# Optimization experiments

Measured on AMD Instinct MI355X. Metric: run time of the kernel, lower is better.

Reference implementation:

```python
import jax, jax.numpy as jnp
import numpy as np

B, S, D_IN, HID, H, OUT = 4, 2048, 1024, 1024, 16, 128
DH = HID // H
SCALE = float(np.sqrt(DH))
ELEV, FLOOR2 = 4, 32


def setup_inputs() -> dict:
    key = jax.random.key(0)
    ks = jax.random.split(key, 12)
    w = lambda k, o, i: jax.random.normal(k, (o, i), dtype=jnp.float32) * 0.02
    b = lambda k, o: jax.random.normal(k, (o,), dtype=jnp.float32) * 0.02
    return {
        "query": jax.random.normal(ks[0], (B, S, D_IN), dtype=jnp.float32),
        "key": jax.random.normal(ks[1], (B, S, D_IN), dtype=jnp.float32),
        "value": jax.random.normal(ks[2], (B, S, D_IN), dtype=jnp.float32),
        "mask": jax.random.randint(ks[3], (B, 1, 1, S), 0, 2, dtype=jnp.int32),
        "wq_w": w(ks[4], HID, D_IN), "wq_b": b(ks[5], HID),
        "wk_w": w(ks[6], HID, D_IN), "wk_b": b(ks[7], HID),
        "wv_w": w(ks[8], HID, D_IN), "wv_b": b(ks[9], HID),
        "fc_w": w(ks[10], OUT, HID), "fc_b": b(ks[11], OUT),
    }


def reference(query, key, value, mask, wq_w, wq_b, wk_w, wk_b, wv_w, wv_b, fc_w, fc_b):
    bsz, seq = query.shape[0], query.shape[1]
    # torch Linear: x @ W.T + b
    split = lambda x: x.reshape(bsz, seq, H, DH).transpose(0, 2, 1, 3)  # (b,h,s,dh)
    Q = split(query @ wq_w.T + wq_b)
    K = split(key @ wk_w.T + wk_b)
    V = split(value @ wv_w.T + wv_b)
    energy = jnp.einsum('bhqd,bhkd->bhqk', Q, K) / SCALE
    energy = jnp.where(mask == 0, jnp.float32(-1e10), energy)
    attn = jax.nn.softmax(energy, axis=-1)  # dropout is identity in eval mode
    x = jnp.einsum('bhqk,bhkd->bhqd', attn, V)
    x = x.transpose(0, 2, 1, 3).reshape(bsz, seq, HID)
    x = x @ fc_w.T + fc_b
    x = x.reshape(-1, ELEV, FLOOR2)  # (b*s, elevator_num, floor_num*2)
    return jax.nn.softmax(x, axis=1)  # nn.Softmax(dim=1)
```

## Files before the change

### kernel.cpp

```cpp
#include <hip/hip_runtime.h>
#include <stdint.h>

#define S_LEN 2048
#define DK 1024
#define NH 16
#define DH 64
#define LOG2E 1.4426950408889634f
#define M_FIX 10.0f

typedef __attribute__((ext_vector_type(8))) short bf16x8;
typedef __attribute__((ext_vector_type(4))) float f32x4;

__device__ __forceinline__ unsigned short f2bf(float f) {
    union { float f; uint32_t u; } v; v.f = f;
    return (unsigned short)((v.u + 0x7fffu + ((v.u >> 16) & 1u)) >> 16);
}

__device__ __forceinline__ float fast_exp2(float x) {
#if __has_builtin(__builtin_amdgcn_exp2f)
    return __builtin_amdgcn_exp2f(x);
#else
    return exp2f(x);
#endif
}

__device__ __forceinline__ uint32_t cvt_pk_bf16(float a, float b) {
    uint32_t r;
    asm("v_cvt_pk_bf16_f32 %0, %1, %2" : "=v"(r) : "v"(a), "v"(b));
    return r;
}

__device__ __forceinline__ void gload_lds16(const void* g, void* l) {
    __builtin_amdgcn_global_load_lds((const __attribute__((address_space(1))) void*)g,
                                     (__attribute__((address_space(3))) void*)l, 16, 0, 0);
}

__global__ __launch_bounds__(256) void cvt3_kernel(
    const float* __restrict__ a0, const float* __restrict__ a1, const float* __restrict__ a2,
    unsigned short* __restrict__ o0, unsigned short* __restrict__ o1, unsigned short* __restrict__ o2,
    int n4)
{
    const float* in = (blockIdx.y == 0) ? a0 : ((blockIdx.y == 1) ? a1 : a2);
    unsigned short* out = (blockIdx.y == 0) ? o0 : ((blockIdx.y == 1) ? o1 : o2);
    const float4* pin = (const float4*)in;
    ushort4* pout = (ushort4*)out;
    int i = blockIdx.x * blockDim.x + threadIdx.x;
    int stride = gridDim.x * blockDim.x;
    for (; i < n4; i += stride) {
        float4 v = pin[i];
        ushort4 o;
        o.x = f2bf(v.x); o.y = f2bf(v.y); o.z = f2bf(v.z); o.w = f2bf(v.w);
        pout[i] = o;
    }
}

__global__ __launch_bounds__(256) void cvt4_kernel(
    const float* __restrict__ a0, const float* __restrict__ a1,
    const float* __restrict__ a2, const float* __restrict__ a3,
    unsigned short* __restrict__ o0, unsigned short* __restrict__ o1,
    unsigned short* __restrict__ o2, unsigned short* __restrict__ o3,
    int n4_012, int n4_3)
{
    const int y = blockIdx.y;
    const float* in = (y == 0) ? a0 : ((y == 1) ? a1 : ((y == 2) ? a2 : a3));
    unsigned short* out = (y == 0) ? o0 : ((y == 1) ? o1 : ((y == 2) ? o2 : o3));
    const int n4 = (y == 3) ? n4_3 : n4_012;
    const float4* pin = (const float4*)in;
    ushort4* pout = (ushort4*)out;
    int i = blockIdx.x * blockDim.x + threadIdx.x;
    int stride = gridDim.x * blockDim.x;
    for (; i < n4; i += stride) {
        float4 v = pin[i];
        ushort4 o;
        o.x = f2bf(v.x); o.y = f2bf(v.y); o.z = f2bf(v.z); o.w = f2bf(v.w);
        pout[i] = o;
    }
}

__global__ __launch_bounds__(256) void proj_gemm(
    const unsigned short* __restrict__ Xq, const unsigned short* __restrict__ Xk, const unsigned short* __restrict__ Xv,
    const unsigned short* __restrict__ Wq, const unsigned short* __restrict__ Wk, const unsigned short* __restrict__ Wv,
    const float* __restrict__ bq, const float* __restrict__ bk, const float* __restrict__ bv,
    unsigned short* __restrict__ Qh, unsigned short* __restrict__ Kh, unsigned short* __restrict__ Vt)
{
    const int d = blockIdx.x + (blockIdx.y << 3) + (blockIdx.z << 9);
    const int k = d & 7, s = d >> 3;
    const int nn = s & 7;
    const int mz = ((s >> 3) << 3) + k;
    const int m0 = (mz & 63) * 128;
    const int z = mz >> 6;

    const unsigned short* X = (z == 0) ? Xq : ((z == 1) ? Xk : Xv);
    const unsigned short* W = (z == 0) ? Wq : ((z == 1) ? Wk : Wv);
    const float* bias = (z == 0) ? bq : ((z == 1) ? bk : bv);

    const int n0 = nn * 128;
    const int tid = threadIdx.x;
    const int w = tid >> 6;
    const int l = tid & 63;
    const int wm = w >> 1, wn = w & 1;
    const int g = l >> 4, c = l & 15;

    __shared__ __align__(16) unsigned short As[3][128 * 32];
    __shared__ __align__(16) unsigned short Bs[3][128 * 32];

    f32x4 acc[4][4] = {};

    const int srow = l >> 2;
    const int schunk = (((l & 3) - (l >> 3)) & 3) * 8;

    auto stage = [&](int kk, int buf) {
#pragma unroll
        for (int j = 0; j < 2; ++j) {
            int r0 = 32 * w + 16 * j;
            gload_lds16(X + (size_t)(m0 + r0 + srow) * DK + kk + schunk, &As[buf][r0 * 32]);
            gload_lds16(W + (size_t)(n0 + r0 + srow) * DK + kk + schunk, &Bs[buf][r0 * 32]);
        }
    };

    stage(0, 0);
    stage(32, 1);

    int cur = 0;
    for (int step = 0; step < 32; ++step) {
        if (step < 31) asm volatile("s_waitcnt vmcnt(4)" ::: "memory");
        else           asm volatile("s_waitcnt vmcnt(0)" ::: "memory");
        __builtin_amdgcn_s_barrier();
        __builtin_amdgcn_sched_barrier(0);

        if (step < 30) {
            int nb = cur + 2; if (nb >= 3) nb -= 3;
            stage((step + 2) << 5, nb);
        }

        bf16x8 a[4], bb[4];
        const int rchunk = 8 * ((g + (c >> 1)) & 3);
#pragma unroll
        for (int mi = 0; mi < 4; ++mi)
            a[mi] = *(const bf16x8*)&As[cur][(64 * wm + 16 * mi + c) * 32 + rchunk];
#pragma unroll
        for (int nj = 0; nj < 4; ++nj)
            bb[nj] = *(const bf16x8*)&Bs[cur][(64 * wn + 16 * nj + c) * 32 + rchunk];
        __builtin_amdgcn_s_setprio(1);
#pragma unroll
        for (int mi = 0; mi < 4; ++mi)
#pragma unroll
            for (int nj = 0; nj < 4; ++nj)
                acc[mi][nj] = __builtin_amdgcn_mfma_f32_16x16x32_bf16(a[mi], bb[nj], acc[mi][nj], 0, 0, 0);
        __builtin_amdgcn_s_setprio(0);

        ++cur; if (cur == 3) cur = 0;
    }

    const float scale = (z == 0) ? 0.125f : 1.0f;
#pragma unroll
    for (int mi = 0; mi < 4; ++mi) {
#pragma unroll
        for (int nj = 0; nj < 4; ++nj) {
            int col = n0 + 64 * wn + 16 * nj + c;
            float bval = bias[col];
            int h = col >> 6, dh = col & 63;
            int row0 = m0 + 64 * wm + 16 * mi + 4 * g;
            int b = row0 >> 11, ss = row0 & 2047;
            if (z != 2) {
                unsigned short* Out = (z == 0) ? Qh : Kh;
#pragma unroll
                for (int r = 0; r < 4; ++r) {
                    float v = (acc[mi][nj][r] + bval) * scale;
                    Out[((size_t)(b * NH + h) * S_LEN + (ss + r)) * DH + dh] = f2bf(v);
                }
            } else {
                ushort4 o;
                o.x = f2bf(acc[mi][nj][0] + bval);
                o.y = f2bf(acc[mi][nj][1] + bval);
                o.z = f2bf(acc[mi][nj][2] + bval);
                o.w = f2bf(acc[mi][nj][3] + bval);
                int q = (ss >> 2) & 7;
                int newpos = (ss & ~31) + 8 * (q & 3) + 4 * (q >> 2);
                *(ushort4*)&Vt[((size_t)(b * NH + h) * DH + dh) * S_LEN + newpos] = o;
            }
        }
    }
}

__global__ __launch_bounds__(256, 5) void attn_kernel(
    const unsigned short* __restrict__ Qh, const unsigned short* __restrict__ Kh,
    const unsigned short* __restrict__ Vt, const int* __restrict__ maskI,
    unsigned short* __restrict__ O)
{
    const int id = blockIdx.x + (blockIdx.y << 4);
    const int swzid = (id & 7) * 128 + (id >> 3);
    const int q0 = (swzid & 15) * 128;
    const int bh = swzid >> 4;
    const int b = bh >> 4, h = bh & 15;
    const int tid = threadIdx.x, w = tid >> 6, l = tid & 63;
    const int g = l >> 4, c = l & 15;

    __shared__ __align__(16) unsigned short Ks[2][32 * 64];
    __shared__ __align__(16) unsigned short Vs[2][64 * 32];
    __shared__ __align__(16) float mskA[S_LEN];

    bf16x8 qf[2][2];
    const size_t qbase = (size_t)bh * S_LEN + q0 + 32 * w;
#pragma unroll
    for (int mi = 0; mi < 2; ++mi)
#pragma unroll
        for (int k32 = 0; k32 < 2; ++k32)
            qf[mi][k32] = *(const bf16x8*)&Qh[(qbase + 16 * mi + c) * DH + k32 * 32 + 8 * g];

    f32x4 ao[2][4] = {};
    f32x4 ls[2] = {};
    bf16x8 ones;
#pragma unroll
    for (int j = 0; j < 8; ++j) ones[j] = (short)0x3F80;

    const int kswz = ((l & 7) ^ (l >> 3)) * 8;
    const int vrow = l >> 2;
    const int vsrc = (((l & 3) - (l >> 3)) & 3) * 8;

    gload_lds16(Kh + ((size_t)bh * S_LEN + 8 * w + (l >> 3)) * DH + kswz, &Ks[0][w * 512]);
    gload_lds16(Vt + ((size_t)bh * DH + 16 * w + vrow) * S_LEN + vsrc, &Vs[0][w * 512]);
    {
        const int4* mp = (const int4*)(maskI + b * S_LEN);
#pragma unroll
        for (int i = 0; i < 2; ++i) {
            int idx = tid + 256 * i;
            int4 m = mp[idx];
            float4 f;
            f.x = m.x ? (-M_FIX * LOG2E) : -3e38f;
            f.y = m.y ? (-M_FIX * LOG2E) : -3e38f;
            f.z = m.z ? (-M_FIX * LOG2E) : -3e38f;
            f.w = m.w ? (-M_FIX * LOG2E) : -3e38f;
            *(float4*)&mskA[idx * 4] = f;
        }
    }

    for (int t = 0; t < 64; ++t) {
        const int cur = t & 1;
        const int kv0 = t << 5;
        __syncthreads();

        if (t < 63) {
            int kvn = kv0 + 32;
            gload_lds16(Kh + ((size_t)bh * S_LEN + kvn + 8 * w + (l >> 3)) * DH + kswz, &Ks[cur ^ 1][w * 512]);
            gload_lds16(Vt + ((size_t)bh * DH + 16 * w + vrow) * S_LEN + kvn + vsrc, &Vs[cur ^ 1][w * 512]);
        }

        f32x4 sf[2][2] = {};
        __builtin_amdgcn_s_setprio(1);
#pragma unroll
        for (int nj = 0; nj < 2; ++nj) {
            int krow = 16 * nj + c;
#pragma unroll
            for (int k32 = 0; k32 < 2; ++k32) {
                int chunk = (k32 * 4 + g) ^ (krow & 7);
                bf16x8 kf = *(const bf16x8*)&Ks[cur][krow * 64 + chunk * 8];
#pragma unroll
                for (int mi = 0; mi < 2; ++mi)
                    sf[mi][nj] = __builtin_amdgcn_mfma_f32_16x16x32_bf16(kf, qf[mi][k32], sf[mi][nj], 0, 0, 0);
            }
        }
        __builtin_amdgcn_s_setprio(0);

        float4 mk0 = *(const float4*)&mskA[kv0 + 4 * g];
        float4 mk1 = *(const float4*)&mskA[kv0 + 16 + 4 * g];
        bf16x8 pf[2];
#pragma unroll
        for (int mi = 0; mi < 2; ++mi) {
            float e00 = fast_exp2(fmaf(sf[mi][0][0], LOG2E, mk0.x));
            float e01 = fast_exp2(fmaf(sf[mi][0][1], LOG2E, mk0.y));
            float e02 = fast_exp2(fmaf(sf[mi][0][2], LOG2E, mk0.z));
            float e03 = fast_exp2(fmaf(sf[mi][0][3], LOG2E, mk0.w));
            float e10 = fast_exp2(fmaf(sf[mi][1][0], LOG2E, mk1.x));
            float e11 = fast_exp2(fmaf(sf[mi][1][1], LOG2E, mk1.y));
            float e12 = fast_exp2(fmaf(sf[mi][1][2], LOG2E, mk1.z));
            float e13 = fast_exp2(fmaf(sf[mi][1][3], LOG2E, mk1.w));
            union { uint32_t u[4]; bf16x8 v; } pu;
            pu.u[0] = cvt_pk_bf16(e00, e01);
            pu.u[1] = cvt_pk_bf16(e02, e03);
            pu.u[2] = cvt_pk_bf16(e10, e11);
            pu.u[3] = cvt_pk_bf16(e12, e13);
            pf[mi] = pu.v;
        }

        __builtin_amdgcn_s_setprio(1);
#pragma unroll
        for (int nc = 0; nc < 4; ++nc) {
            int row = 16 * nc + c;
            int s16 = (g + (c >> 1)) & 3;
            bf16x8 vf = *(const bf16x8*)&Vs[cur][row * 32 + 8 * s16];
#pragma unroll
            for (int mi = 0; mi < 2; ++mi)
                ao[mi][nc] = __builtin_amdgcn_mfma_f32_16x16x32_bf16(pf[mi], vf, ao[mi][nc], 0, 0, 0);
        }
#pragma unroll
        for (int mi = 0; mi < 2; ++mi)
            ls[mi] = __builtin_amdgcn_mfma_f32_16x16x32_bf16(pf[mi], ones, ls[mi], 0, 0, 0);
        __builtin_amdgcn_s_setprio(0);
    }

#pragma unroll
    for (int mi = 0; mi < 2; ++mi)
#pragma unroll
        for (int r = 0; r < 4; ++r) {
            int s = q0 + 32 * w + 16 * mi + 4 * g + r;
            float inv = 1.0f / ls[mi][r];
#pragma unroll
            for (int nc = 0; nc < 4; ++nc) {
                int dh = 16 * nc + c;
                O[(size_t)(b * S_LEN + s) * 1024 + h * DH + dh] = f2bf(ao[mi][nc][r] * inv);
            }
        }
}

__global__ __launch_bounds__(256) void fc_kernel(
    const unsigned short* __restrict__ O, const unsigned short* __restrict__ Wf,
    const float* __restrict__ bfc, float* __restrict__ out)
{
    const int m0 = blockIdx.x * 64;
    const int tid = threadIdx.x, w = tid >> 6, l = tid & 63;
    const int g = l >> 4, c = l & 15;

    __shared__ __align__(16) unsigned short As[3][64 * 32];
    __shared__ __align__(16) unsigned short Bs[3][128 * 32];

    f32x4 acc[8] = {};

    const int srow = l >> 2;
    const int schunk = (((l & 3) - (l >> 3)) & 3) * 8;

    auto stage = [&](int kk, int buf) {
        gload_lds16(O + (size_t)(m0 + 16 * w + srow) * DK + kk + schunk, &As[buf][16 * w * 32]);
#pragma unroll
        for (int j = 0; j < 2; ++j) {
            int r0 = 32 * w + 16 * j;
            gload_lds16(Wf + (size_t)(r0 + srow) * DK + kk + schunk, &Bs[buf][r0 * 32]);
        }
    };

    stage(0, 0);
    stage(32, 1);

    int cur = 0;
    for (int step = 0; step < 32; ++step) {
        if (step < 31) asm volatile("s_waitcnt vmcnt(3)" ::: "memory");
        else           asm volatile("s_waitcnt vmcnt(0)" ::: "memory");
        __builtin_amdgcn_s_barrier();
        __builtin_amdgcn_sched_barrier(0);

        if (step < 30) {
            int nb = cur + 2; if (nb >= 3) nb -= 3;
            stage((step + 2) << 5, nb);
        }

        const int rchunk = 8 * ((g + (c >> 1)) & 3);
        bf16x8 a = *(const bf16x8*)&As[cur][(16 * w + c) * 32 + rchunk];
        bf16x8 bb[8];
#pragma unroll
        for (int nj = 0; nj < 8; ++nj)
            bb[nj] = *(const bf16x8*)&Bs[cur][(16 * nj + c) * 32 + rchunk];
        __builtin_amdgcn_s_setprio(1);
#pragma unroll
        for (int nj = 0; nj < 8; ++nj)
            acc[nj] = __builtin_amdgcn_mfma_f32_16x16x32_bf16(a, bb[nj], acc[nj], 0, 0, 0);
        __builtin_amdgcn_s_setprio(0);

        ++cur; if (cur == 3) cur = 0;
    }

#pragma unroll
    for (int r = 0; r < 4; ++r) {
        int row = m0 + 16 * w + (l >> 4) * 4 + r;
#pragma unroll
        for (int par = 0; par < 2; ++par) {
            float v[4];
#pragma unroll
            for (int e = 0; e < 4; ++e) {
                int col = 16 * (2 * e + par) + (l & 15);
                v[e] = acc[2 * e + par][r] + bfc[col];
            }
            float mx = fmaxf(fmaxf(v[0], v[1]), fmaxf(v[2], v[3]));
            float ex[4], ssum = 0.f;
#pragma unroll
            for (int e = 0; e < 4; ++e) { ex[e] = fast_exp2((v[e] - mx) * LOG2E); ssum += ex[e]; }
            float inv = 1.0f / ssum;
#pragma unroll
            for (int e = 0; e < 4; ++e) {
                int col = 16 * (2 * e + par) + (l & 15);
                out[(size_t)row * 128 + col] = ex[e] * inv;
            }
        }
    }
}

extern "C" void kernel_launch(void* const* d_in, const int* in_sizes, int n_in,
                              void* d_out, int out_size, void* d_ws, size_t ws_size,
                              hipStream_t stream) {
    (void)in_sizes; (void)n_in; (void)out_size; (void)ws_size;
    const float* q    = (const float*)d_in[0];
    const float* k    = (const float*)d_in[1];
    const float* v    = (const float*)d_in[2];
    const int*   mask = (const int*)d_in[3];
    const float* wq_w = (const float*)d_in[4];
    const float* wq_b = (const float*)d_in[5];
    const float* wk_w = (const float*)d_in[6];
    const float* wk_b = (const float*)d_in[7];
    const float* wv_w = (const float*)d_in[8];
    const float* wv_b = (const float*)d_in[9];
    const float* fc_w = (const float*)d_in[10];
    const float* fc_b = (const float*)d_in[11];

    const size_t NX = (size_t)8192 * 1024;
    const size_t NW = (size_t)1024 * 1024;
    const size_t NF = (size_t)128 * 1024;

    unsigned short* Xq = (unsigned short*)d_ws;
    unsigned short* Xk = Xq + NX;
    unsigned short* Xv = Xk + NX;
    unsigned short* Wq = Xv + NX;
    unsigned short* Wk = Wq + NW;
    unsigned short* Wv = Wk + NW;
    unsigned short* Wf = Wv + NW;
    unsigned short* Qh = Wf + NF;
    unsigned short* Kh = Qh + NX;
    unsigned short* Vt = Kh + NX;
    unsigned short* O  = Xq;

    cvt3_kernel<<<dim3(2048, 3), 256, 0, stream>>>(q, k, v, Xq, Xk, Xv, (int)(NX / 4));
    cvt4_kernel<<<dim3(512, 4), 256, 0, stream>>>(wq_w, wk_w, wv_w, fc_w,
                                                  Wq, Wk, Wv, Wf,
                                                  (int)(NW / 4), (int)(NF / 4));

    proj_gemm<<<dim3(8, 64, 3), 256, 0, stream>>>(Xq, Xk, Xv, Wq, Wk, Wv,
                                                  wq_b, wk_b, wv_b, Qh, Kh, Vt);
    attn_kernel<<<dim3(16, 64), 256, 0, stream>>>(Qh, Kh, Vt, mask, O);
    fc_kernel<<<128, 256, 0, stream>>>(O, Wf, fc_b, (float*)d_out);
}
```

Before: 195.2 us.

## Merge conversion kernels, shrink B staging, and fold log2e and mask into MFMA

Three independent changes. The two fp32-to-bf16 conversion launches become one 7-slice launch, removing a kernel launch and its tail. In the projection GEMM the weight tile is double-buffered instead of triple-buffered and prefetched one step ahead, which cuts LDS use at the cost of a shallower prefetch for B. The Q projection now folds log2(e) into its scale and the attention kernel seeds the MFMA accumulator with the mask bias, so the per-element fma before exp2 goes away; slightly different rounding of Q in bf16 is the tradeoff.

```diff
diff --git a/kernel.cpp b/kernel.cpp
--- a/kernel.cpp
+++ b/kernel.cpp
@@ -35,36 +35,21 @@
                                      (__attribute__((address_space(3))) void*)l, 16, 0, 0);
 }
 
-__global__ __launch_bounds__(256) void cvt3_kernel(
+__global__ __launch_bounds__(256) void cvt7_kernel(
     const float* __restrict__ a0, const float* __restrict__ a1, const float* __restrict__ a2,
+    const float* __restrict__ a3, const float* __restrict__ a4, const float* __restrict__ a5,
+    const float* __restrict__ a6,
     unsigned short* __restrict__ o0, unsigned short* __restrict__ o1, unsigned short* __restrict__ o2,
-    int n4)
-{
-    const float* in = (blockIdx.y == 0) ? a0 : ((blockIdx.y == 1) ? a1 : a2);
-    unsigned short* out = (blockIdx.y == 0) ? o0 : ((blockIdx.y == 1) ? o1 : o2);
-    const float4* pin = (const float4*)in;
-    ushort4* pout = (ushort4*)out;
-    int i = blockIdx.x * blockDim.x + threadIdx.x;
-    int stride = gridDim.x * blockDim.x;
-    for (; i < n4; i += stride) {
-        float4 v = pin[i];
-        ushort4 o;
-        o.x = f2bf(v.x); o.y = f2bf(v.y); o.z = f2bf(v.z); o.w = f2bf(v.w);
-        pout[i] = o;
-    }
-}
-
-__global__ __launch_bounds__(256) void cvt4_kernel(
-    const float* __restrict__ a0, const float* __restrict__ a1,
-    const float* __restrict__ a2, const float* __restrict__ a3,
-    unsigned short* __restrict__ o0, unsigned short* __restrict__ o1,
-    unsigned short* __restrict__ o2, unsigned short* __restrict__ o3,
-    int n4_012, int n4_3)
+    unsigned short* __restrict__ o3, unsigned short* __restrict__ o4, unsigned short* __restrict__ o5,
+    unsigned short* __restrict__ o6,
+    int n4_big, int n4_w, int n4_f)
 {
     const int y = blockIdx.y;
-    const float* in = (y == 0) ? a0 : ((y == 1) ? a1 : ((y == 2) ? a2 : a3));
-    unsigned short* out = (y == 0) ? o0 : ((y == 1) ? o1 : ((y == 2) ? o2 : o3));
-    const int n4 = (y == 3) ? n4_3 : n4_012;
+    const float* in = (y == 0) ? a0 : (y == 1) ? a1 : (y == 2) ? a2 :
+                      (y == 3) ? a3 : (y == 4) ? a4 : (y == 5) ? a5 : a6;
+    unsigned short* out = (y == 0) ? o0 : (y == 1) ? o1 : (y == 2) ? o2 :
+                          (y == 3) ? o3 : (y == 4) ? o4 : (y == 5) ? o5 : o6;
+    const int n4 = (y < 3) ? n4_big : ((y < 6) ? n4_w : n4_f);
     const float4* pin = (const float4*)in;
     ushort4* pout = (ushort4*)out;
     int i = blockIdx.x * blockDim.x + threadIdx.x;
@@ -102,45 +87,53 @@
     const int g = l >> 4, c = l & 15;
 
     __shared__ __align__(16) unsigned short As[3][128 * 32];
-    __shared__ __align__(16) unsigned short Bs[3][128 * 32];
+    __shared__ __align__(16) unsigned short Bs[2][128 * 32];
 
     f32x4 acc[4][4] = {};
 
     const int srow = l >> 2;
     const int schunk = (((l & 3) - (l >> 3)) & 3) * 8;
 
-    auto stage = [&](int kk, int buf) {
+    auto stageA = [&](int kk, int buf) {
 #pragma unroll
         for (int j = 0; j < 2; ++j) {
             int r0 = 32 * w + 16 * j;
             gload_lds16(X + (size_t)(m0 + r0 + srow) * DK + kk + schunk, &As[buf][r0 * 32]);
+        }
+    };
+    auto stageB = [&](int kk, int buf) {
+#pragma unroll
+        for (int j = 0; j < 2; ++j) {
+            int r0 = 32 * w + 16 * j;
             gload_lds16(W + (size_t)(n0 + r0 + srow) * DK + kk + schunk, &Bs[buf][r0 * 32]);
         }
     };
 
-    stage(0, 0);
-    stage(32, 1);
-
-    int cur = 0;
+    stageA(0, 0);
+    stageB(0, 0);
+    stageA(32, 1);
+
+    int curA = 0;
     for (int step = 0; step < 32; ++step) {
-        if (step < 31) asm volatile("s_waitcnt vmcnt(4)" ::: "memory");
+        if (step < 31) asm volatile("s_waitcnt vmcnt(2)" ::: "memory");
         else           asm volatile("s_waitcnt vmcnt(0)" ::: "memory");
         __builtin_amdgcn_s_barrier();
         __builtin_amdgcn_sched_barrier(0);
 
+        if (step < 31) stageB((step + 1) << 5, (step + 1) & 1);
         if (step < 30) {
-            int nb = cur + 2; if (nb >= 3) nb -= 3;
-            stage((step + 2) << 5, nb);
+            int nb = curA + 2; if (nb >= 3) nb -= 3;
+            stageA((step + 2) << 5, nb);
         }
 
         bf16x8 a[4], bb[4];
         const int rchunk = 8 * ((g + (c >> 1)) & 3);
 #pragma unroll
         for (int mi = 0; mi < 4; ++mi)
-            a[mi] = *(const bf16x8*)&As[cur][(64 * wm + 16 * mi + c) * 32 + rchunk];
+            a[mi] = *(const bf16x8*)&As[curA][(64 * wm + 16 * mi + c) * 32 + rchunk];
 #pragma unroll
         for (int nj = 0; nj < 4; ++nj)
-            bb[nj] = *(const bf16x8*)&Bs[cur][(64 * wn + 16 * nj + c) * 32 + rchunk];
+            bb[nj] = *(const bf16x8*)&Bs[step & 1][(64 * wn + 16 * nj + c) * 32 + rchunk];
         __builtin_amdgcn_s_setprio(1);
 #pragma unroll
         for (int mi = 0; mi < 4; ++mi)
@@ -149,10 +142,10 @@
                 acc[mi][nj] = __builtin_amdgcn_mfma_f32_16x16x32_bf16(a[mi], bb[nj], acc[mi][nj], 0, 0, 0);
         __builtin_amdgcn_s_setprio(0);
 
-        ++cur; if (cur == 3) cur = 0;
-    }
-
-    const float scale = (z == 0) ? 0.125f : 1.0f;
+        ++curA; if (curA == 3) curA = 0;
+    }
+
+    const float scale = (z == 0) ? (0.125f * LOG2E) : 1.0f;
 #pragma unroll
     for (int mi = 0; mi < 4; ++mi) {
 #pragma unroll
@@ -246,7 +239,14 @@
             gload_lds16(Vt + ((size_t)bh * DH + 16 * w + vrow) * S_LEN + kvn + vsrc, &Vs[cur ^ 1][w * 512]);
         }
 
-        f32x4 sf[2][2] = {};
+        float4 mk0 = *(const float4*)&mskA[kv0 + 4 * g];
+        float4 mk1 = *(const float4*)&mskA[kv0 + 16 + 4 * g];
+        f32x4 sf[2][2];
+        sf[0][0] = f32x4{mk0.x, mk0.y, mk0.z, mk0.w};
+        sf[1][0] = sf[0][0];
+        sf[0][1] = f32x4{mk1.x, mk1.y, mk1.z, mk1.w};
+        sf[1][1] = sf[0][1];
+
         __builtin_amdgcn_s_setprio(1);
 #pragma unroll
         for (int nj = 0; nj < 2; ++nj) {
@@ -262,19 +262,17 @@
         }
         __builtin_amdgcn_s_setprio(0);
 
-        float4 mk0 = *(const float4*)&mskA[kv0 + 4 * g];
-        float4 mk1 = *(const float4*)&mskA[kv0 + 16 + 4 * g];
         bf16x8 pf[2];
 #pragma unroll
         for (int mi = 0; mi < 2; ++mi) {
-            float e00 = fast_exp2(fmaf(sf[mi][0][0], LOG2E, mk0.x));
-            float e01 = fast_exp2(fmaf(sf[mi][0][1], LOG2E, mk0.y));
-            float e02 = fast_exp2(fmaf(sf[mi][0][2], LOG2E, mk0.z));
-            float e03 = fast_exp2(fmaf(sf[mi][0][3], LOG2E, mk0.w));
-            float e10 = fast_exp2(fmaf(sf[mi][1][0], LOG2E, mk1.x));
-            float e11 = fast_exp2(fmaf(sf[mi][1][1], LOG2E, mk1.y));
-            float e12 = fast_exp2(fmaf(sf[mi][1][2], LOG2E, mk1.z));
-            float e13 = fast_exp2(fmaf(sf[mi][1][3], LOG2E, mk1.w));
+            float e00 = fast_exp2(sf[mi][0][0]);
+            float e01 = fast_exp2(sf[mi][0][1]);
+            float e02 = fast_exp2(sf[mi][0][2]);
+            float e03 = fast_exp2(sf[mi][0][3]);
+            float e10 = fast_exp2(sf[mi][1][0]);
+            float e11 = fast_exp2(sf[mi][1][1]);
+            float e12 = fast_exp2(sf[mi][1][2]);
+            float e13 = fast_exp2(sf[mi][1][3]);
             union { uint32_t u[4]; bf16x8 v; } pu;
             pu.u[0] = cvt_pk_bf16(e00, e01);
             pu.u[1] = cvt_pk_bf16(e02, e03);
@@ -426,10 +424,9 @@
     unsigned short* Vt = Kh + NX;
     unsigned short* O  = Xq;
 
-    cvt3_kernel<<<dim3(2048, 3), 256, 0, stream>>>(q, k, v, Xq, Xk, Xv, (int)(NX / 4));
-    cvt4_kernel<<<dim3(512, 4), 256, 0, stream>>>(wq_w, wk_w, wv_w, fc_w,
-                                                  Wq, Wk, Wv, Wf,
-                                                  (int)(NW / 4), (int)(NF / 4));
+    cvt7_kernel<<<dim3(2048, 7), 256, 0, stream>>>(q, k, v, wq_w, wk_w, wv_w, fc_w,
+                                                   Xq, Xk, Xv, Wq, Wk, Wv, Wf,
+                                                   (int)(NX / 4), (int)(NW / 4), (int)(NF / 4));
 
     proj_gemm<<<dim3(8, 64, 3), 256, 0, stream>>>(Xq, Xk, Xv, Wq, Wk, Wv,
                                                   wq_b, wk_b, wv_b, Qh, Kh, Vt);
```

Result: faster. 190.5 us (-2.4%).
